# Performance work log

Measured on AMD Instinct MI355X. Metric: run time of the kernel, lower is better.

The kernel has to match this reference:

```python
import jax, jax.numpy as jnp
import numpy as np
import math

B, L, DIM = 2, 2048, 1024
NUM_HEADS, QUANTUM_HEADS, CHUNK = 16, 2, 64
HD = DIM // NUM_HEADS  # 64 == CHUNK (required by the original broadcast)
TH = NUM_HEADS - QUANTUM_HEADS
STEPS = 2048
LN_EPS = 1e-5


def setup_inputs() -> dict:
    key = jax.random.key(0)
    ks = jax.random.split(key, 12)
    inp = {
        'x': jax.random.normal(ks[0], (B, L, DIM), dtype=jnp.float32),
        # to_quantum_state: Linear(HD, 2HD) + LayerNorm(2HD) + Tanh
        'wq1': jax.random.normal(ks[1], (HD, 2 * HD), dtype=jnp.float32) * 0.05,
        'bq1': jnp.zeros((2 * HD,), dtype=jnp.float32),
        'ln_g': jnp.ones((2 * HD,), dtype=jnp.float32),
        'ln_b': jnp.zeros((2 * HD,), dtype=jnp.float32),
        'phase_shifts': jax.random.normal(ks[2], (QUANTUM_HEADS,), dtype=jnp.float32) * 0.02,
        'freqs': jax.random.normal(ks[3], (QUANTUM_HEADS,), dtype=jnp.float32) * 0.02,
        # traditional heads: q/k/v projections, no bias
        'wq': jax.random.normal(ks[4], (DIM, TH * HD), dtype=jnp.float32) * 0.02,
        'wk': jax.random.normal(ks[5], (DIM, TH * HD), dtype=jnp.float32) * 0.02,
        'wv': jax.random.normal(ks[6], (DIM, TH * HD), dtype=jnp.float32) * 0.02,
        # output projection
        'wo': jax.random.normal(ks[7], (DIM, DIM), dtype=jnp.float32) * 0.02,
        'bo': jnp.zeros((DIM,), dtype=jnp.float32),
    }
    return inp


def _quantum_state(t, wq1, bq1, ln_g, ln_b):
    # Linear -> LayerNorm -> Tanh; split into (amp, phase)
    h = t @ wq1 + bq1
    mu = h.mean(-1, keepdims=True)
    var = ((h - mu) ** 2).mean(-1, keepdims=True)
    h = (h - mu) * jax.lax.rsqrt(var + LN_EPS) * ln_g + ln_b
    h = jnp.tanh(h)
    return h[..., :HD], h[..., HD:]


def reference(x, wq1, bq1, ln_g, ln_b, phase_shifts, freqs, wq, wk, wv, wo, bo):
    two_pi = 2.0 * math.pi
    angles = jnp.linspace(0.0, two_pi, STEPS)  # torch.linspace is endpoint-inclusive
    cos_table = jnp.cos(angles)
    inv_sqrt_hd = 1.0 / math.sqrt(HD)
    nc = L // CHUNK

    quantum_outs = []
    for h in range(QUANTUM_HEADS):
        xh = x[..., h * HD:(h + 1) * HD]                       # [B,L,HD]
        amp, phase = _quantum_state(xh, wq1, bq1, ln_g, ln_b)  # each [B,L,HD]
        qa = amp.reshape(B, nc, CHUNK, HD)
        qp = phase.reshape(B, nc, CHUNK, HD)
        # keys/values are truncated to the FIRST `chunk` tokens (original quirk)
        ka = amp[:, :CHUNK]        # [B,CHUNK,HD]
        kp = phase[:, :CHUNK]
        v = xh[:, :CHUNK]
        # phase_diff[b,c,i,j] = qp[b,c,i,j] - kp[b,j,i]  (needs CHUNK == HD)
        pd = (qp - jnp.swapaxes(kp, -1, -2)[:, None]) * freqs[h] + phase_shifts[h]
        idx = jnp.mod(pd / two_pi * STEPS, STEPS).astype(jnp.int32)  # in [0, STEPS)
        interference = cos_table[idx]                          # [B,nc,CHUNK,CHUNK]
        scores = jnp.einsum('bcih,bjh->bcij', qa, ka) * interference
        attn = jax.nn.softmax(scores * inv_sqrt_hd, axis=-1)
        out = jnp.einsum('bcij,bjh->bcih', attn, v).reshape(B, L, HD)
        quantum_outs.append(out)

    # traditional multi-head attention on full x
    q = (x @ wq).reshape(B, L, TH, HD)
    k = (x @ wk).reshape(B, L, TH, HD)
    vv = (x @ wv).reshape(B, L, TH, HD)
    scores = jnp.einsum('bqhd,bkhd->bhqk', q, k) * inv_sqrt_hd
    attn = jax.nn.softmax(scores, axis=-1)
    trad = jnp.einsum('bhqk,bkhd->bqhd', attn, vv).reshape(B, L, TH * HD)

    out = jnp.concatenate(quantum_outs + [trad], axis=-1)  # [B,L,DIM]
    return out @ wo + bo
```

## Files before the change

kernel.cpp:

```cpp
#include <hip/hip_runtime.h>
#include <hip/hip_bf16.h>
#include <math.h>

#define B_ 2
#define L_ 2048
#define DIM_ 1024
#define HD_ 64
#define TH_ 14
#define TWO_PI_F 6.28318530717958647692f
#define QSCALE_F 0.1803368801111204f

typedef __bf16 bf16_t;
typedef __bf16 bf16x8 __attribute__((ext_vector_type(8)));
typedef __bf16 bf16x4 __attribute__((ext_vector_type(4)));
typedef float f32x4 __attribute__((ext_vector_type(4)));
typedef float f32x16 __attribute__((ext_vector_type(16)));
typedef unsigned int u32x2 __attribute__((ext_vector_type(2)));

static __device__ __forceinline__ bf16_t f2b(float f) { return (bf16_t)f; }

static __device__ __forceinline__ float fexp2(float x) {
#if __has_builtin(__builtin_amdgcn_exp2f)
  return __builtin_amdgcn_exp2f(x);
#else
  return exp2f(x);
#endif
}

static __device__ __forceinline__ unsigned int cvtpk(float a, float b) {
  unsigned int r;
  asm("v_cvt_pk_bf16_f32 %0, %1, %2" : "=v"(r) : "v"(a), "v"(b));
  return r;
}

static __device__ __forceinline__ void gl16(const bf16_t* g, bf16_t* l) {
  __builtin_amdgcn_global_load_lds(
      (const __attribute__((address_space(1))) void*)g,
      (__attribute__((address_space(3))) void*)l, 16, 0, 0);
}

static __device__ __forceinline__ void swap32(unsigned int& a, unsigned int& b) {
#if __has_builtin(__builtin_amdgcn_permlane32_swap)
  u32x2 r = __builtin_amdgcn_permlane32_swap(a, b, false, false);
  a = r[0];
  b = r[1];
#else
  const int l = (int)(threadIdx.x & 63);
  unsigned int bp_a = (unsigned int)__builtin_amdgcn_ds_bpermute((l ^ 32) << 2, (int)a);
  unsigned int bp_b = (unsigned int)__builtin_amdgcn_ds_bpermute((l ^ 32) << 2, (int)b);
  unsigned int na = (l < 32) ? a : bp_b;
  unsigned int nb = (l < 32) ? bp_a : b;
  a = na;
  b = nb;
#endif
}

__global__ __launch_bounds__(256)
void k_prep(const float* __restrict__ x, const float* __restrict__ wq1,
            const float* __restrict__ bq1, const float* __restrict__ ln_g,
            const float* __restrict__ ln_b, const float* __restrict__ wq,
            const float* __restrict__ wk, const float* __restrict__ wv,
            const float* __restrict__ wo, bf16_t* __restrict__ xb,
            bf16_t* __restrict__ wt_qkv, bf16_t* __restrict__ wt_o,
            bf16_t* __restrict__ amp_b, float* __restrict__ phase) {
  __shared__ float tile[32][33];
  const int t = threadIdx.x;
  const int bid = blockIdx.x;
  if (bid < 4096) {
    const int i = bid * 256 + t;
    const float4 v4 = ((const float4*)x)[i];
    bf16x4 o = {f2b(v4.x), f2b(v4.y), f2b(v4.z), f2b(v4.w)};
    *(bf16x4*)(xb + 4 * (size_t)i) = o;
  } else if (bid < 7808) {
    const float* W;
    bf16_t* Wt;
    int N, kt, nt;
    if (bid < 6784) {
      int r = bid - 4096;
      const int which = r / 896;
      r -= which * 896;
      W = (which == 0) ? wq : (which == 1) ? wk : wv;
      Wt = wt_qkv + (size_t)which * 896 * 1024;
      N = 896;
      kt = r & 31;
      nt = r >> 5;
    } else {
      const int r = bid - 6784;
      W = wo;
      Wt = wt_o;
      N = 1024;
      kt = r & 31;
      nt = r >> 5;
    }
    const int tx = t & 31, ty = t >> 5;
    const int k0 = kt * 32, n0 = nt * 32;
    #pragma unroll
    for (int i = 0; i < 4; ++i)
      tile[ty + 8 * i][tx] = W[(size_t)(k0 + ty + 8 * i) * N + n0 + tx];
    __syncthreads();
    #pragma unroll
    for (int i = 0; i < 4; ++i)
      Wt[(size_t)(n0 + ty + 8 * i) * 1024 + k0 + tx] = f2b(tile[tx][ty + 8 * i]);
  } else {
    const int gw = ((bid - 7808) * 256 + t) >> 6;
    const int lane = t & 63;
    const int h = gw >> 12;
    const int bl = gw & 4095;
    const float xv = x[(size_t)bl * DIM_ + h * HD_ + lane];
    float acc0 = bq1[lane];
    float acc1 = bq1[64 + lane];
    #pragma unroll 16
    for (int kk = 0; kk < 64; ++kk) {
      const float xk = __shfl(xv, kk, 64);
      acc0 = fmaf(xk, wq1[kk * 128 + lane], acc0);
      acc1 = fmaf(xk, wq1[kk * 128 + 64 + lane], acc1);
    }
    float s = acc0 + acc1;
    #pragma unroll
    for (int off = 32; off > 0; off >>= 1) s += __shfl_xor(s, off, 64);
    const float mu = s * (1.0f / 128.0f);
    const float d0 = acc0 - mu, d1 = acc1 - mu;
    float vsum = d0 * d0 + d1 * d1;
    #pragma unroll
    for (int off = 32; off > 0; off >>= 1) vsum += __shfl_xor(vsum, off, 64);
    const float rstd = rsqrtf(vsum * (1.0f / 128.0f) + 1e-5f);
    const float av = tanhf(d0 * rstd * ln_g[lane] + ln_b[lane]);
    const float pv = tanhf(d1 * rstd * ln_g[64 + lane] + ln_b[64 + lane]);
    const size_t o = ((size_t)h * (B_ * L_) + bl) * HD_ + lane;
    amp_b[o] = f2b(av);
    phase[o] = pv;
  }
}

__global__ __launch_bounds__(256)
void k_mm1q(const bf16_t* __restrict__ A, const bf16_t* __restrict__ Wt,
            bf16_t* __restrict__ qb, bf16_t* __restrict__ kb, bf16_t* __restrict__ vb,
            const bf16_t* __restrict__ amp_b, const float* __restrict__ phase,
            const float* __restrict__ shifts, const float* __restrict__ freqs,
            bf16_t* __restrict__ catb) {
  __shared__ char smem[32768];
  const int t = threadIdx.x;
  const int lane = t & 63, w = t >> 6;
  const int bid = blockIdx.x;
  const int xcd = bid & 7, slot = bid >> 3;
  if (slot < 84) {
    bf16_t* Asm = (bf16_t*)smem;
    bf16_t* Bsm = (bf16_t*)(smem + 16384);
    const int wm = w >> 1, wn = w & 1;
    const int l31 = lane & 31, hi = lane >> 5;
    const int m_blk = xcd * 4 + slot / 21;
    const int n_blk = slot % 21;
    const int m0 = m_blk * 128;
    const int n0 = n_blk * 128;
    f32x16 acc[2][2] = {};
    for (int k0 = 0; k0 < 1024; k0 += 64) {
      __syncthreads();
      #pragma unroll
      for (int qc = 0; qc < 4; ++qc) {
        const int idx = t + 256 * qc;
        const int r = idx >> 3, cb = idx & 7;
        const int c = (cb ^ (r & 7)) * 8;
        gl16(A + (size_t)(m0 + r) * 1024 + k0 + c, Asm + w * 512 + qc * 2048);
        gl16(Wt + (size_t)(n0 + r) * 1024 + k0 + c, Bsm + w * 512 + qc * 2048);
      }
      __syncthreads();
      #pragma unroll
      for (int s = 0; s < 4; ++s) {
        const int ra0 = wm * 64 + l31, ra1 = ra0 + 32;
        const int rb0 = wn * 64 + l31, rb1 = rb0 + 32;
        const bf16x8 af0 = *(const bf16x8*)((char*)Asm + ra0 * 128 + (((2 * s + hi) ^ (ra0 & 7)) << 4));
        const bf16x8 af1 = *(const bf16x8*)((char*)Asm + ra1 * 128 + (((2 * s + hi) ^ (ra1 & 7)) << 4));
        const bf16x8 bf0 = *(const bf16x8*)((char*)Bsm + rb0 * 128 + (((2 * s + hi) ^ (rb0 & 7)) << 4));
        const bf16x8 bf1 = *(const bf16x8*)((char*)Bsm + rb1 * 128 + (((2 * s + hi) ^ (rb1 & 7)) << 4));
        acc[0][0] = __builtin_amdgcn_mfma_f32_32x32x16_bf16(bf0, af0, acc[0][0], 0, 0, 0);
        acc[0][1] = __builtin_amdgcn_mfma_f32_32x32x16_bf16(bf1, af0, acc[0][1], 0, 0, 0);
        acc[1][0] = __builtin_amdgcn_mfma_f32_32x32x16_bf16(bf0, af1, acc[1][0], 0, 0, 0);
        acc[1][1] = __builtin_amdgcn_mfma_f32_32x32x16_bf16(bf1, af1, acc[1][1], 0, 0, 0);
      }
    }
    const int n0w = n0 + wn * 64;
    const int which = (n0 >= 1792) ? 2 : (n0 >= 896) ? 1 : 0;
    #pragma unroll
    for (int mi = 0; mi < 2; ++mi) {
      const int m = m0 + wm * 64 + mi * 32 + l31;
      const int bsel = m >> 11, ll = m & 2047;
      #pragma unroll
      for (int ni = 0; ni < 2; ++ni) {
        if (which == 2) {
          #pragma unroll
          for (int rp = 0; rp < 4; ++rp) {
            #pragma unroll
            for (int e = 0; e < 4; ++e) {
              const int nn = n0w + ni * 32 + 8 * rp + 4 * hi + e - 1792;
              const int head = nn >> 6, hd = nn & 63;
              vb[(((size_t)bsel * TH_ + head) * HD_ + hd) * L_ + ll] = f2b(acc[mi][ni][4 * rp + e]);
            }
          }
        } else {
          const float sc = (which == 0) ? QSCALE_F : 1.0f;
          bf16_t* dst = (which == 0) ? qb : kb;
          #pragma unroll
          for (int rp = 0; rp < 4; ++rp) {
            const int nb = n0w + ni * 32 + 8 * rp + 4 * hi;
            const int nn = nb - which * 896;
            const int head = nn >> 6, hd = nn & 63;
            bf16x4 pk;
            #pragma unroll
            for (int e = 0; e < 4; ++e) pk[e] = f2b(acc[mi][ni][4 * rp + e] * sc);
            *(bf16x4*)(dst + (((size_t)bsel * TH_ + head) * L_ + ll) * HD_ + hd) = pk;
          }
        }
      }
    }
  } else {
    bf16_t* Kam = (bf16_t*)smem;
    bf16_t* Vt  = (bf16_t*)(smem + 8192);
    bf16_t* Ps  = (bf16_t*)(smem + 16384);
    const int l15 = lane & 15, g = lane >> 4;
    const int qv = xcd * 16 + (slot - 84);
    const int c = qv & 31;
    const int hb = qv >> 5;
    const int b = hb & 1;
    const int h = hb >> 1;
    const size_t abase = ((size_t)h * B_ + b) * L_ * HD_;

    {
      const int r0 = t >> 3, cb0 = t & 7;
      const int r1 = r0 + 32;
      gl16(amp_b + abase + r0 * 64 + (cb0 ^ (r0 & 7)) * 8, Kam + w * 512);
      gl16(amp_b + abase + r1 * 64 + (cb0 ^ (r1 & 7)) * 8, Kam + w * 512 + 2048);
    }
    {
      const int vj = t >> 2;
      const int vd0 = (t & 3) * 16;
      const bf16x8 va = *(const bf16x8*)(A + ((size_t)b * L_ + vj) * DIM_ + h * 64 + vd0);
      const bf16x8 vb2 = *(const bf16x8*)(A + ((size_t)b * L_ + vj) * DIM_ + h * 64 + vd0 + 8);
      #pragma unroll
      for (int e = 0; e < 8; ++e) {
        int d = vd0 + e;
        *(bf16_t*)((char*)Vt + d * 128 + (((vj >> 3) ^ (d & 7)) << 4) + (vj & 7) * 2) = va[e];
        d = vd0 + 8 + e;
        *(bf16_t*)((char*)Vt + d * 128 + (((vj >> 3) ^ (d & 7)) << 4) + (vj & 7) * 2) = vb2[e];
      }
    }
    __syncthreads();

    bf16x8 qf[2];
    {
      const size_t ro = abase + (size_t)(c * 64 + 16 * w + l15) * 64 + g * 8;
      qf[0] = *(const bf16x8*)(amp_b + ro);
      qf[1] = *(const bf16x8*)(amp_b + ro + 32);
    }
    f32x4 s[4] = {};
    #pragma unroll
    for (int ks = 0; ks < 2; ++ks) {
      #pragma unroll
      for (int nt = 0; nt < 4; ++nt) {
        const int jr = nt * 16 + l15;
        const bf16x8 kf = *(const bf16x8*)((char*)Kam + jr * 128 + (((ks * 4 + g) ^ (jr & 7)) << 4));
        s[nt] = __builtin_amdgcn_mfma_f32_16x16x32_bf16(qf[ks], kf, s[nt], 0, 0, 0);
      }
    }
    const float freq = freqs[h], shift = shifts[h];
    char* PsW = (char*)Ps + w * 2048;
    float l_acc[4];
    #pragma unroll
    for (int r = 0; r < 4; ++r) {
      const int i_loc = 16 * w + 4 * g + r;
      const float* qrow = phase + abase + (size_t)(c * 64 + i_loc) * 64;
      const float* krow = phase + abase + i_loc;
      const int row = g * 4 + r;
      float ls = 0.0f;
      #pragma unroll
      for (int nt = 0; nt < 4; ++nt) {
        const int j = nt * 16 + l15;
        const float qp = qrow[j];
        const float kp = krow[j * 64];
        const float pd = (qp - kp) * freq + shift;
        const float t1 = pd * (2048.0f / TWO_PI_F);
        float mm = fmodf(t1, 2048.0f);
        if (mm < 0.0f) mm += 2048.0f;
        int idx = (int)mm;
        idx = idx > 2047 ? 2047 : idx;
        const float interf = cosf((float)idx * (TWO_PI_F / 2047.0f));
        const float sc = s[nt][r] * interf * 0.125f;
        const float e = expf(sc);
        ls += e;
        *(bf16_t*)(PsW + row * 128 + (((j >> 3) ^ (row & 7)) << 4) + (j & 7) * 2) = f2b(e);
      }
      #pragma unroll
      for (int off = 1; off < 16; off <<= 1) ls += __shfl_xor(ls, off, 64);
      l_acc[r] = ls;
    }
    f32x4 o[4] = {};
    #pragma unroll
    for (int ks = 0; ks < 2; ++ks) {
      const bf16x8 pa = *(const bf16x8*)(PsW + l15 * 128 + (((ks * 4 + g) ^ (l15 & 7)) << 4));
      #pragma unroll
      for (int nt = 0; nt < 4; ++nt) {
        const int dr = nt * 16 + l15;
        const bf16x8 vf = *(const bf16x8*)((char*)Vt + dr * 128 + (((ks * 4 + g) ^ (dr & 7)) << 4));
        o[nt] = __builtin_amdgcn_mfma_f32_16x16x32_bf16(pa, vf, o[nt], 0, 0, 0);
      }
    }
    #pragma unroll
    for (int r = 0; r < 4; ++r) {
      const float inv = 1.0f / l_acc[r];
      const int qrow = c * 64 + 16 * w + g * 4 + r;
      #pragma unroll
      for (int nt = 0; nt < 4; ++nt)
        catb[((size_t)b * L_ + qrow) * DIM_ + h * 64 + nt * 16 + l15] = f2b(o[nt][r] * inv);
    }
  }
}

__global__ __launch_bounds__(256)
void k_mm0(const bf16_t* __restrict__ A, const bf16_t* __restrict__ Wt,
           const float* __restrict__ bias, float* __restrict__ outf) {
  __shared__ bf16_t Asm[128 * 64];
  __shared__ bf16_t Bsm[128 * 64];
  const int t = threadIdx.x;
  const int lane = t & 63, w = t >> 6;
  const int wm = w >> 1, wn = w & 1;
  const int l31 = lane & 31, hi = lane >> 5;
  const int bid = blockIdx.x;
  const int v = (bid & 7) * 32 + (bid >> 3);
  const int m0 = (v & 31) * 128;
  const int n0 = (v >> 5) * 128;
  f32x16 acc[2][2] = {};
  for (int k0 = 0; k0 < 1024; k0 += 64) {
    __syncthreads();
    #pragma unroll
    for (int qc = 0; qc < 4; ++qc) {
      const int idx = t + 256 * qc;
      const int r = idx >> 3, cb = idx & 7;
      const int c = (cb ^ (r & 7)) * 8;
      gl16(A + (size_t)(m0 + r) * 1024 + k0 + c, Asm + w * 512 + qc * 2048);
      gl16(Wt + (size_t)(n0 + r) * 1024 + k0 + c, Bsm + w * 512 + qc * 2048);
    }
    __syncthreads();
    #pragma unroll
    for (int s = 0; s < 4; ++s) {
      const int ra0 = wm * 64 + l31, ra1 = ra0 + 32;
      const int rb0 = wn * 64 + l31, rb1 = rb0 + 32;
      const bf16x8 af0 = *(const bf16x8*)((char*)Asm + ra0 * 128 + (((2 * s + hi) ^ (ra0 & 7)) << 4));
      const bf16x8 af1 = *(const bf16x8*)((char*)Asm + ra1 * 128 + (((2 * s + hi) ^ (ra1 & 7)) << 4));
      const bf16x8 bf0 = *(const bf16x8*)((char*)Bsm + rb0 * 128 + (((2 * s + hi) ^ (rb0 & 7)) << 4));
      const bf16x8 bf1 = *(const bf16x8*)((char*)Bsm + rb1 * 128 + (((2 * s + hi) ^ (rb1 & 7)) << 4));
      acc[0][0] = __builtin_amdgcn_mfma_f32_32x32x16_bf16(bf0, af0, acc[0][0], 0, 0, 0);
      acc[0][1] = __builtin_amdgcn_mfma_f32_32x32x16_bf16(bf1, af0, acc[0][1], 0, 0, 0);
      acc[1][0] = __builtin_amdgcn_mfma_f32_32x32x16_bf16(bf0, af1, acc[1][0], 0, 0, 0);
      acc[1][1] = __builtin_amdgcn_mfma_f32_32x32x16_bf16(bf1, af1, acc[1][1], 0, 0, 0);
    }
  }
  #pragma unroll
  for (int mi = 0; mi < 2; ++mi) {
    const int m = m0 + wm * 64 + mi * 32 + l31;
    #pragma unroll
    for (int ni = 0; ni < 2; ++ni) {
      #pragma unroll
      for (int rp = 0; rp < 4; ++rp) {
        const int nb = n0 + wn * 64 + ni * 32 + 8 * rp + 4 * hi;
        const float4 bv = *(const float4*)&bias[nb];
        float4 r4;
        r4.x = acc[mi][ni][4 * rp + 0] + bv.x;
        r4.y = acc[mi][ni][4 * rp + 1] + bv.y;
        r4.z = acc[mi][ni][4 * rp + 2] + bv.z;
        r4.w = acc[mi][ni][4 * rp + 3] + bv.w;
        *(float4*)&outf[(size_t)m * 1024 + nb] = r4;
      }
    }
  }
}

__global__ __launch_bounds__(512)
void k_flash2(const bf16_t* __restrict__ qg, const bf16_t* __restrict__ kg,
              const bf16_t* __restrict__ vt, bf16_t* __restrict__ catb) {
  __shared__ char smem[65536];
  const int t = threadIdx.x;
  const int lane = t & 63, w = t >> 6;
  const int g2 = w >> 2, wl = w & 3;
  const int l31 = lane & 31, hi = lane >> 5;
  int bid = blockIdx.x;
  bid = (bid & 7) * 56 + (bid >> 3);
  const int qblk = bid & 15, bh = bid >> 4;
  const int head = bh % TH_, b = bh / TH_;
  const size_t base = (size_t)bh * (L_ * HD_);
  const int q = qblk * 128 + wl * 32 + l31;
  const int tl = t & 255;
  const int r0 = tl >> 3, cb0 = tl & 7;
  const int r1 = r0 + 32;
  const int c0 = (cb0 ^ (r0 & 7)) * 8;
  const int c1 = (cb0 ^ (r1 & 7)) * 8;
  const int ubase = wl * 512;
  bf16_t* Kg = (bf16_t*)(smem + g2 * 32768);
  bf16_t* Vg = (bf16_t*)(smem + g2 * 32768 + 16384);
  const int kt0 = g2 * 16;

  bf16x8 qf[4];
  #pragma unroll
  for (int slot = 0; slot < 4; ++slot)
    qf[slot] = *(const bf16x8*)(qg + base + (size_t)q * 64 + 16 * slot + 8 * hi);

  f32x16 oT[2] = {};
  float l_acc = 0.0f;

  {
    const bf16_t* ksrc = kg + base + (size_t)kt0 * 64 * 64;
    const bf16_t* vsrc = vt + base + kt0 * 64;
    gl16(ksrc + r0 * 64 + c0, Kg + ubase);
    gl16(ksrc + r1 * 64 + c1, Kg + ubase + 2048);
    gl16(vsrc + (size_t)r0 * L_ + c0, Vg + ubase);
    gl16(vsrc + (size_t)r1 * L_ + c1, Vg + ubase + 2048);
  }
  for (int kt = 0; kt < 16; ++kt) {
    const int cur = kt & 1;
    if (kt < 15) {
      const bf16_t* ksrc = kg + base + (size_t)(kt0 + kt + 1) * 64 * 64;
      const bf16_t* vsrc = vt + base + (kt0 + kt + 1) * 64;
      bf16_t* kd = Kg + (cur ^ 1) * 4096;
      bf16_t* vd = Vg + (cur ^ 1) * 4096;
      gl16(ksrc + r0 * 64 + c0, kd + ubase);
      gl16(ksrc + r1 * 64 + c1, kd + ubase + 2048);
      gl16(vsrc + (size_t)r0 * L_ + c0, vd + ubase);
      gl16(vsrc + (size_t)r1 * L_ + c1, vd + ubase + 2048);
      asm volatile("s_waitcnt vmcnt(4)" ::: "memory");
    } else {
      asm volatile("s_waitcnt vmcnt(0)" ::: "memory");
    }
    __builtin_amdgcn_sched_barrier(0);
    __builtin_amdgcn_s_barrier();
    const char* Kc = (const char*)(Kg + cur * 4096);
    const char* Vc = (const char*)(Vg + cur * 4096);
    f32x16 sT0 = {}, sT1 = {};
    __builtin_amdgcn_s_setprio(1);
    #pragma unroll
    for (int slot = 0; slot < 4; ++slot) {
      const int row0 = l31;
      const int row1 = 32 + l31;
      const bf16x8 kf0 = *(const bf16x8*)(Kc + row0 * 128 + (((2 * slot + hi) ^ (row0 & 7)) << 4));
      const bf16x8 kf1 = *(const bf16x8*)(Kc + row1 * 128 + (((2 * slot + hi) ^ (row1 & 7)) << 4));
      sT0 = __builtin_amdgcn_mfma_f32_32x32x16_bf16(kf0, qf[slot], sT0, 0, 0, 0);
      sT1 = __builtin_amdgcn_mfma_f32_32x32x16_bf16(kf1, qf[slot], sT1, 0, 0, 0);
    }
    __builtin_amdgcn_s_setprio(0);
    unsigned int W0[8], W1[8];
    float la = 0.0f;
    #pragma unroll
    for (int rp = 0; rp < 8; ++rp) {
      const float p00 = fexp2(sT0[2 * rp]);
      const float p01 = fexp2(sT0[2 * rp + 1]);
      const float p10 = fexp2(sT1[2 * rp]);
      const float p11 = fexp2(sT1[2 * rp + 1]);
      la += (p00 + p01) + (p10 + p11);
      W0[rp] = cvtpk(p00, p01);
      W1[rp] = cvtpk(p10, p11);
    }
    l_acc += la;
    unsigned int pb[4][4];
    #pragma unroll
    for (int m1 = 0; m1 < 2; ++m1) {
      unsigned int u, vv;
      u = W0[m1];     vv = W0[2 + m1]; swap32(u, vv); pb[0][m1] = u; pb[0][m1 + 2] = vv;
      u = W0[4 + m1]; vv = W0[6 + m1]; swap32(u, vv); pb[1][m1] = u; pb[1][m1 + 2] = vv;
      u = W1[m1];     vv = W1[2 + m1]; swap32(u, vv); pb[2][m1] = u; pb[2][m1 + 2] = vv;
      u = W1[4 + m1]; vv = W1[6 + m1]; swap32(u, vv); pb[3][m1] = u; pb[3][m1 + 2] = vv;
    }
    __builtin_amdgcn_s_setprio(1);
    #pragma unroll
    for (int slot = 0; slot < 4; ++slot) {
      union { unsigned int u[4]; bf16x8 v8; } pf;
      pf.u[0] = pb[slot][0]; pf.u[1] = pb[slot][1];
      pf.u[2] = pb[slot][2]; pf.u[3] = pb[slot][3];
      #pragma unroll
      for (int dt = 0; dt < 2; ++dt) {
        const int row = 32 * dt + l31;
        const bf16x8 vf = *(const bf16x8*)(Vc + row * 128 + (((2 * slot + hi) ^ (row & 7)) << 4));
        oT[dt] = __builtin_amdgcn_mfma_f32_32x32x16_bf16(vf, pf.v8, oT[dt], 0, 0, 0);
      }
    }
    __builtin_amdgcn_s_setprio(0);
    __builtin_amdgcn_s_barrier();
  }
  const float l_w = l_acc + __shfl_xor(l_acc, 32, 64);
  __syncthreads();
  float* obuf = (float*)(smem + 32768);
  float* lbuf = (float*)smem;
  if (g2 == 1) {
    #pragma unroll
    for (int dt = 0; dt < 2; ++dt)
      #pragma unroll
      for (int e = 0; e < 16; ++e)
        obuf[(dt * 16 + e) * 256 + wl * 64 + lane] = oT[dt][e];
    lbuf[wl * 64 + lane] = l_w;
  }
  __syncthreads();
  if (g2 == 0) {
    const float l_tot = l_w + lbuf[wl * 64 + lane];
    const float inv = 1.0f / l_tot;
    const size_t obase = ((size_t)b * L_ + q) * DIM_ + 128 + head * 64;
    #pragma unroll
    for (int dt = 0; dt < 2; ++dt) {
      #pragma unroll
      for (int rq = 0; rq < 4; ++rq) {
        bf16x4 pk;
        #pragma unroll
        for (int e = 0; e < 4; ++e)
          pk[e] = f2b((oT[dt][4 * rq + e] +
                       obuf[(dt * 16 + 4 * rq + e) * 256 + wl * 64 + lane]) * inv);
        *(bf16x4*)(catb + obase + 32 * dt + 8 * rq + 4 * hi) = pk;
      }
    }
  }
}

extern "C" void kernel_launch(void* const* d_in, const int* in_sizes, int n_in,
                              void* d_out, int out_size, void* d_ws, size_t ws_size,
                              hipStream_t stream) {
  (void)in_sizes; (void)n_in; (void)out_size; (void)ws_size;
  const float* x      = (const float*)d_in[0];
  const float* wq1    = (const float*)d_in[1];
  const float* bq1    = (const float*)d_in[2];
  const float* ln_g   = (const float*)d_in[3];
  const float* ln_b   = (const float*)d_in[4];
  const float* shifts = (const float*)d_in[5];
  const float* freqs  = (const float*)d_in[6];
  const float* wq     = (const float*)d_in[7];
  const float* wk     = (const float*)d_in[8];
  const float* wv     = (const float*)d_in[9];
  const float* wo     = (const float*)d_in[10];
  const float* bo     = (const float*)d_in[11];
  float* out = (float*)d_out;

  char* p = (char*)d_ws;
  bf16_t* amp_b  = (bf16_t*)p; p += (size_t)2 * B_ * L_ * HD_ * 2;
  float* phase   = (float*)p;  p += (size_t)2 * B_ * L_ * HD_ * 4;
  bf16_t* xb     = (bf16_t*)p; p += (size_t)B_ * L_ * DIM_ * 2;
  bf16_t* wt_qkv = (bf16_t*)p; p += (size_t)2688 * 1024 * 2;
  bf16_t* wt_o   = (bf16_t*)p; p += (size_t)1024 * 1024 * 2;
  bf16_t* qb     = (bf16_t*)p; p += (size_t)B_ * TH_ * L_ * HD_ * 2;
  bf16_t* kb     = (bf16_t*)p; p += (size_t)B_ * TH_ * L_ * HD_ * 2;
  bf16_t* vtb    = (bf16_t*)p; p += (size_t)B_ * TH_ * L_ * HD_ * 2;
  bf16_t* catb   = (bf16_t*)p;

  k_prep<<<dim3(9856), dim3(256), 0, stream>>>(x, wq1, bq1, ln_g, ln_b,
                                               wq, wk, wv, wo,
                                               xb, wt_qkv, wt_o, amp_b, phase);
  k_mm1q<<<dim3(800), dim3(256), 0, stream>>>(xb, wt_qkv, qb, kb, vtb,
                                              amp_b, phase, shifts, freqs, catb);
  k_flash2<<<dim3(448), dim3(512), 0, stream>>>(qb, kb, vtb, catb);
  k_mm0<<<dim3(256), dim3(256), 0, stream>>>(catb, wt_o, bo, out);
}
```

Baseline: 121.0 us.

## Move quantum-head attention blocks from QKV GEMM kernel into flash kernel

The chunked quantum-head attention work, previously run as 128 extra blocks of the QKV projection GEMM kernel, now runs inside the flash-attention kernel as 64 extra 512-thread blocks, each doing two chunks with one 256-thread group per chunk. The GEMM kernel becomes a pure GEMM with 672 blocks, and the flash kernel grows from 448 to 512 blocks. The goal is to rebalance load: the GEMM grid shrinks and the small quantum blocks fill idle CUs during flash attention rather than competing with GEMM tiles. The risk is that quantum blocks in the flash grid occupy 512-thread slots and extend the flash kernel's tail.

```diff
diff --git a/kernel.cpp b/kernel.cpp
--- a/kernel.cpp
+++ b/kernel.cpp
@@ -134,182 +134,78 @@
 
 __global__ __launch_bounds__(256)
 void k_mm1q(const bf16_t* __restrict__ A, const bf16_t* __restrict__ Wt,
-            bf16_t* __restrict__ qb, bf16_t* __restrict__ kb, bf16_t* __restrict__ vb,
-            const bf16_t* __restrict__ amp_b, const float* __restrict__ phase,
-            const float* __restrict__ shifts, const float* __restrict__ freqs,
-            bf16_t* __restrict__ catb) {
+            bf16_t* __restrict__ qb, bf16_t* __restrict__ kb, bf16_t* __restrict__ vb) {
   __shared__ char smem[32768];
   const int t = threadIdx.x;
   const int lane = t & 63, w = t >> 6;
   const int bid = blockIdx.x;
   const int xcd = bid & 7, slot = bid >> 3;
-  if (slot < 84) {
-    bf16_t* Asm = (bf16_t*)smem;
-    bf16_t* Bsm = (bf16_t*)(smem + 16384);
-    const int wm = w >> 1, wn = w & 1;
-    const int l31 = lane & 31, hi = lane >> 5;
-    const int m_blk = xcd * 4 + slot / 21;
-    const int n_blk = slot % 21;
-    const int m0 = m_blk * 128;
-    const int n0 = n_blk * 128;
-    f32x16 acc[2][2] = {};
-    for (int k0 = 0; k0 < 1024; k0 += 64) {
-      __syncthreads();
-      #pragma unroll
-      for (int qc = 0; qc < 4; ++qc) {
-        const int idx = t + 256 * qc;
-        const int r = idx >> 3, cb = idx & 7;
-        const int c = (cb ^ (r & 7)) * 8;
-        gl16(A + (size_t)(m0 + r) * 1024 + k0 + c, Asm + w * 512 + qc * 2048);
-        gl16(Wt + (size_t)(n0 + r) * 1024 + k0 + c, Bsm + w * 512 + qc * 2048);
-      }
-      __syncthreads();
-      #pragma unroll
-      for (int s = 0; s < 4; ++s) {
-        const int ra0 = wm * 64 + l31, ra1 = ra0 + 32;
-        const int rb0 = wn * 64 + l31, rb1 = rb0 + 32;
-        const bf16x8 af0 = *(const bf16x8*)((char*)Asm + ra0 * 128 + (((2 * s + hi) ^ (ra0 & 7)) << 4));
-        const bf16x8 af1 = *(const bf16x8*)((char*)Asm + ra1 * 128 + (((2 * s + hi) ^ (ra1 & 7)) << 4));
-        const bf16x8 bf0 = *(const bf16x8*)((char*)Bsm + rb0 * 128 + (((2 * s + hi) ^ (rb0 & 7)) << 4));
-        const bf16x8 bf1 = *(const bf16x8*)((char*)Bsm + rb1 * 128 + (((2 * s + hi) ^ (rb1 & 7)) << 4));
-        acc[0][0] = __builtin_amdgcn_mfma_f32_32x32x16_bf16(bf0, af0, acc[0][0], 0, 0, 0);
-        acc[0][1] = __builtin_amdgcn_mfma_f32_32x32x16_bf16(bf1, af0, acc[0][1], 0, 0, 0);
-        acc[1][0] = __builtin_amdgcn_mfma_f32_32x32x16_bf16(bf0, af1, acc[1][0], 0, 0, 0);
-        acc[1][1] = __builtin_amdgcn_mfma_f32_32x32x16_bf16(bf1, af1, acc[1][1], 0, 0, 0);
-      }
-    }
-    const int n0w = n0 + wn * 64;
-    const int which = (n0 >= 1792) ? 2 : (n0 >= 896) ? 1 : 0;
-    #pragma unroll
-    for (int mi = 0; mi < 2; ++mi) {
-      const int m = m0 + wm * 64 + mi * 32 + l31;
-      const int bsel = m >> 11, ll = m & 2047;
-      #pragma unroll
-      for (int ni = 0; ni < 2; ++ni) {
-        if (which == 2) {
+  bf16_t* Asm = (bf16_t*)smem;
+  bf16_t* Bsm = (bf16_t*)(smem + 16384);
+  const int wm = w >> 1, wn = w & 1;
+  const int l31 = lane & 31, hi = lane >> 5;
+  const int m_blk = xcd * 4 + slot / 21;
+  const int n_blk = slot % 21;
+  const int m0 = m_blk * 128;
+  const int n0 = n_blk * 128;
+  f32x16 acc[2][2] = {};
+  for (int k0 = 0; k0 < 1024; k0 += 64) {
+    __syncthreads();
+    #pragma unroll
+    for (int qc = 0; qc < 4; ++qc) {
+      const int idx = t + 256 * qc;
+      const int r = idx >> 3, cb = idx & 7;
+      const int c = (cb ^ (r & 7)) * 8;
+      gl16(A + (size_t)(m0 + r) * 1024 + k0 + c, Asm + w * 512 + qc * 2048);
+      gl16(Wt + (size_t)(n0 + r) * 1024 + k0 + c, Bsm + w * 512 + qc * 2048);
+    }
+    __syncthreads();
+    #pragma unroll
+    for (int s = 0; s < 4; ++s) {
+      const int ra0 = wm * 64 + l31, ra1 = ra0 + 32;
+      const int rb0 = wn * 64 + l31, rb1 = rb0 + 32;
+      const bf16x8 af0 = *(const bf16x8*)((char*)Asm + ra0 * 128 + (((2 * s + hi) ^ (ra0 & 7)) << 4));
+      const bf16x8 af1 = *(const bf16x8*)((char*)Asm + ra1 * 128 + (((2 * s + hi) ^ (ra1 & 7)) << 4));
+      const bf16x8 bf0 = *(const bf16x8*)((char*)Bsm + rb0 * 128 + (((2 * s + hi) ^ (rb0 & 7)) << 4));
+      const bf16x8 bf1 = *(const bf16x8*)((char*)Bsm + rb1 * 128 + (((2 * s + hi) ^ (rb1 & 7)) << 4));
+      acc[0][0] = __builtin_amdgcn_mfma_f32_32x32x16_bf16(bf0, af0, acc[0][0], 0, 0, 0);
+      acc[0][1] = __builtin_amdgcn_mfma_f32_32x32x16_bf16(bf1, af0, acc[0][1], 0, 0, 0);
+      acc[1][0] = __builtin_amdgcn_mfma_f32_32x32x16_bf16(bf0, af1, acc[1][0], 0, 0, 0);
+      acc[1][1] = __builtin_amdgcn_mfma_f32_32x32x16_bf16(bf1, af1, acc[1][1], 0, 0, 0);
+    }
+  }
+  const int n0w = n0 + wn * 64;
+  const int which = (n0 >= 1792) ? 2 : (n0 >= 896) ? 1 : 0;
+  #pragma unroll
+  for (int mi = 0; mi < 2; ++mi) {
+    const int m = m0 + wm * 64 + mi * 32 + l31;
+    const int bsel = m >> 11, ll = m & 2047;
+    #pragma unroll
+    for (int ni = 0; ni < 2; ++ni) {
+      if (which == 2) {
+        #pragma unroll
+        for (int rp = 0; rp < 4; ++rp) {
           #pragma unroll
-          for (int rp = 0; rp < 4; ++rp) {
-            #pragma unroll
-            for (int e = 0; e < 4; ++e) {
-              const int nn = n0w + ni * 32 + 8 * rp + 4 * hi + e - 1792;
-              const int head = nn >> 6, hd = nn & 63;
-              vb[(((size_t)bsel * TH_ + head) * HD_ + hd) * L_ + ll] = f2b(acc[mi][ni][4 * rp + e]);
-            }
-          }
-        } else {
-          const float sc = (which == 0) ? QSCALE_F : 1.0f;
-          bf16_t* dst = (which == 0) ? qb : kb;
-          #pragma unroll
-          for (int rp = 0; rp < 4; ++rp) {
-            const int nb = n0w + ni * 32 + 8 * rp + 4 * hi;
-            const int nn = nb - which * 896;
+          for (int e = 0; e < 4; ++e) {
+            const int nn = n0w + ni * 32 + 8 * rp + 4 * hi + e - 1792;
             const int head = nn >> 6, hd = nn & 63;
-            bf16x4 pk;
-            #pragma unroll
-            for (int e = 0; e < 4; ++e) pk[e] = f2b(acc[mi][ni][4 * rp + e] * sc);
-            *(bf16x4*)(dst + (((size_t)bsel * TH_ + head) * L_ + ll) * HD_ + hd) = pk;
+            vb[(((size_t)bsel * TH_ + head) * HD_ + hd) * L_ + ll] = f2b(acc[mi][ni][4 * rp + e]);
           }
         }
-      }
-    }
-  } else {
-    bf16_t* Kam = (bf16_t*)smem;
-    bf16_t* Vt  = (bf16_t*)(smem + 8192);
-    bf16_t* Ps  = (bf16_t*)(smem + 16384);
-    const int l15 = lane & 15, g = lane >> 4;
-    const int qv = xcd * 16 + (slot - 84);
-    const int c = qv & 31;
-    const int hb = qv >> 5;
-    const int b = hb & 1;
-    const int h = hb >> 1;
-    const size_t abase = ((size_t)h * B_ + b) * L_ * HD_;
-
-    {
-      const int r0 = t >> 3, cb0 = t & 7;
-      const int r1 = r0 + 32;
-      gl16(amp_b + abase + r0 * 64 + (cb0 ^ (r0 & 7)) * 8, Kam + w * 512);
-      gl16(amp_b + abase + r1 * 64 + (cb0 ^ (r1 & 7)) * 8, Kam + w * 512 + 2048);
-    }
-    {
-      const int vj = t >> 2;
-      const int vd0 = (t & 3) * 16;
-      const bf16x8 va = *(const bf16x8*)(A + ((size_t)b * L_ + vj) * DIM_ + h * 64 + vd0);
-      const bf16x8 vb2 = *(const bf16x8*)(A + ((size_t)b * L_ + vj) * DIM_ + h * 64 + vd0 + 8);
-      #pragma unroll
-      for (int e = 0; e < 8; ++e) {
-        int d = vd0 + e;
-        *(bf16_t*)((char*)Vt + d * 128 + (((vj >> 3) ^ (d & 7)) << 4) + (vj & 7) * 2) = va[e];
-        d = vd0 + 8 + e;
-        *(bf16_t*)((char*)Vt + d * 128 + (((vj >> 3) ^ (d & 7)) << 4) + (vj & 7) * 2) = vb2[e];
-      }
-    }
-    __syncthreads();
-
-    bf16x8 qf[2];
-    {
-      const size_t ro = abase + (size_t)(c * 64 + 16 * w + l15) * 64 + g * 8;
-      qf[0] = *(const bf16x8*)(amp_b + ro);
-      qf[1] = *(const bf16x8*)(amp_b + ro + 32);
-    }
-    f32x4 s[4] = {};
-    #pragma unroll
-    for (int ks = 0; ks < 2; ++ks) {
-      #pragma unroll
-      for (int nt = 0; nt < 4; ++nt) {
-        const int jr = nt * 16 + l15;
-        const bf16x8 kf = *(const bf16x8*)((char*)Kam + jr * 128 + (((ks * 4 + g) ^ (jr & 7)) << 4));
-        s[nt] = __builtin_amdgcn_mfma_f32_16x16x32_bf16(qf[ks], kf, s[nt], 0, 0, 0);
-      }
-    }
-    const float freq = freqs[h], shift = shifts[h];
-    char* PsW = (char*)Ps + w * 2048;
-    float l_acc[4];
-    #pragma unroll
-    for (int r = 0; r < 4; ++r) {
-      const int i_loc = 16 * w + 4 * g + r;
-      const float* qrow = phase + abase + (size_t)(c * 64 + i_loc) * 64;
-      const float* krow = phase + abase + i_loc;
-      const int row = g * 4 + r;
-      float ls = 0.0f;
-      #pragma unroll
-      for (int nt = 0; nt < 4; ++nt) {
-        const int j = nt * 16 + l15;
-        const float qp = qrow[j];
-        const float kp = krow[j * 64];
-        const float pd = (qp - kp) * freq + shift;
-        const float t1 = pd * (2048.0f / TWO_PI_F);
-        float mm = fmodf(t1, 2048.0f);
-        if (mm < 0.0f) mm += 2048.0f;
-        int idx = (int)mm;
-        idx = idx > 2047 ? 2047 : idx;
-        const float interf = cosf((float)idx * (TWO_PI_F / 2047.0f));
-        const float sc = s[nt][r] * interf * 0.125f;
-        const float e = expf(sc);
-        ls += e;
-        *(bf16_t*)(PsW + row * 128 + (((j >> 3) ^ (row & 7)) << 4) + (j & 7) * 2) = f2b(e);
-      }
-      #pragma unroll
-      for (int off = 1; off < 16; off <<= 1) ls += __shfl_xor(ls, off, 64);
-      l_acc[r] = ls;
-    }
-    f32x4 o[4] = {};
-    #pragma unroll
-    for (int ks = 0; ks < 2; ++ks) {
-      const bf16x8 pa = *(const bf16x8*)(PsW + l15 * 128 + (((ks * 4 + g) ^ (l15 & 7)) << 4));
-      #pragma unroll
-      for (int nt = 0; nt < 4; ++nt) {
-        const int dr = nt * 16 + l15;
-        const bf16x8 vf = *(const bf16x8*)((char*)Vt + dr * 128 + (((ks * 4 + g) ^ (dr & 7)) << 4));
-        o[nt] = __builtin_amdgcn_mfma_f32_16x16x32_bf16(pa, vf, o[nt], 0, 0, 0);
-      }
-    }
-    #pragma unroll
-    for (int r = 0; r < 4; ++r) {
-      const float inv = 1.0f / l_acc[r];
-      const int qrow = c * 64 + 16 * w + g * 4 + r;
-      #pragma unroll
-      for (int nt = 0; nt < 4; ++nt)
-        catb[((size_t)b * L_ + qrow) * DIM_ + h * 64 + nt * 16 + l15] = f2b(o[nt][r] * inv);
+      } else {
+        const float sc = (which == 0) ? QSCALE_F : 1.0f;
+        bf16_t* dst = (which == 0) ? qb : kb;
+        #pragma unroll
+        for (int rp = 0; rp < 4; ++rp) {
+          const int nb = n0w + ni * 32 + 8 * rp + 4 * hi;
+          const int nn = nb - which * 896;
+          const int head = nn >> 6, hd = nn & 63;
+          bf16x4 pk;
+          #pragma unroll
+          for (int e = 0; e < 4; ++e) pk[e] = f2b(acc[mi][ni][4 * rp + e] * sc);
+          *(bf16x4*)(dst + (((size_t)bsel * TH_ + head) * L_ + ll) * HD_ + hd) = pk;
+        }
+      }
     }
   }
 }
@@ -375,141 +271,248 @@
 
 __global__ __launch_bounds__(512)
 void k_flash2(const bf16_t* __restrict__ qg, const bf16_t* __restrict__ kg,
-              const bf16_t* __restrict__ vt, bf16_t* __restrict__ catb) {
+              const bf16_t* __restrict__ vt, bf16_t* __restrict__ catb,
+              const bf16_t* __restrict__ A, const bf16_t* __restrict__ amp_b,
+              const float* __restrict__ phase, const float* __restrict__ shifts,
+              const float* __restrict__ freqs) {
   __shared__ char smem[65536];
   const int t = threadIdx.x;
   const int lane = t & 63, w = t >> 6;
-  const int g2 = w >> 2, wl = w & 3;
   const int l31 = lane & 31, hi = lane >> 5;
-  int bid = blockIdx.x;
-  bid = (bid & 7) * 56 + (bid >> 3);
-  const int qblk = bid & 15, bh = bid >> 4;
-  const int head = bh % TH_, b = bh / TH_;
-  const size_t base = (size_t)bh * (L_ * HD_);
-  const int q = qblk * 128 + wl * 32 + l31;
-  const int tl = t & 255;
-  const int r0 = tl >> 3, cb0 = tl & 7;
-  const int r1 = r0 + 32;
-  const int c0 = (cb0 ^ (r0 & 7)) * 8;
-  const int c1 = (cb0 ^ (r1 & 7)) * 8;
-  const int ubase = wl * 512;
-  bf16_t* Kg = (bf16_t*)(smem + g2 * 32768);
-  bf16_t* Vg = (bf16_t*)(smem + g2 * 32768 + 16384);
-  const int kt0 = g2 * 16;
-
-  bf16x8 qf[4];
-  #pragma unroll
-  for (int slot = 0; slot < 4; ++slot)
-    qf[slot] = *(const bf16x8*)(qg + base + (size_t)q * 64 + 16 * slot + 8 * hi);
-
-  f32x16 oT[2] = {};
-  float l_acc = 0.0f;
-
-  {
-    const bf16_t* ksrc = kg + base + (size_t)kt0 * 64 * 64;
-    const bf16_t* vsrc = vt + base + kt0 * 64;
-    gl16(ksrc + r0 * 64 + c0, Kg + ubase);
-    gl16(ksrc + r1 * 64 + c1, Kg + ubase + 2048);
-    gl16(vsrc + (size_t)r0 * L_ + c0, Vg + ubase);
-    gl16(vsrc + (size_t)r1 * L_ + c1, Vg + ubase + 2048);
-  }
-  for (int kt = 0; kt < 16; ++kt) {
-    const int cur = kt & 1;
-    if (kt < 15) {
-      const bf16_t* ksrc = kg + base + (size_t)(kt0 + kt + 1) * 64 * 64;
-      const bf16_t* vsrc = vt + base + (kt0 + kt + 1) * 64;
-      bf16_t* kd = Kg + (cur ^ 1) * 4096;
-      bf16_t* vd = Vg + (cur ^ 1) * 4096;
-      gl16(ksrc + r0 * 64 + c0, kd + ubase);
-      gl16(ksrc + r1 * 64 + c1, kd + ubase + 2048);
-      gl16(vsrc + (size_t)r0 * L_ + c0, vd + ubase);
-      gl16(vsrc + (size_t)r1 * L_ + c1, vd + ubase + 2048);
-      asm volatile("s_waitcnt vmcnt(4)" ::: "memory");
-    } else {
-      asm volatile("s_waitcnt vmcnt(0)" ::: "memory");
-    }
-    __builtin_amdgcn_sched_barrier(0);
-    __builtin_amdgcn_s_barrier();
-    const char* Kc = (const char*)(Kg + cur * 4096);
-    const char* Vc = (const char*)(Vg + cur * 4096);
-    f32x16 sT0 = {}, sT1 = {};
-    __builtin_amdgcn_s_setprio(1);
-    #pragma unroll
-    for (int slot = 0; slot < 4; ++slot) {
-      const int row0 = l31;
-      const int row1 = 32 + l31;
-      const bf16x8 kf0 = *(const bf16x8*)(Kc + row0 * 128 + (((2 * slot + hi) ^ (row0 & 7)) << 4));
-      const bf16x8 kf1 = *(const bf16x8*)(Kc + row1 * 128 + (((2 * slot + hi) ^ (row1 & 7)) << 4));
-      sT0 = __builtin_amdgcn_mfma_f32_32x32x16_bf16(kf0, qf[slot], sT0, 0, 0, 0);
-      sT1 = __builtin_amdgcn_mfma_f32_32x32x16_bf16(kf1, qf[slot], sT1, 0, 0, 0);
-    }
-    __builtin_amdgcn_s_setprio(0);
-    unsigned int W0[8], W1[8];
-    float la = 0.0f;
-    #pragma unroll
-    for (int rp = 0; rp < 8; ++rp) {
-      const float p00 = fexp2(sT0[2 * rp]);
-      const float p01 = fexp2(sT0[2 * rp + 1]);
-      const float p10 = fexp2(sT1[2 * rp]);
-      const float p11 = fexp2(sT1[2 * rp + 1]);
-      la += (p00 + p01) + (p10 + p11);
-      W0[rp] = cvtpk(p00, p01);
-      W1[rp] = cvtpk(p10, p11);
-    }
-    l_acc += la;
-    unsigned int pb[4][4];
-    #pragma unroll
-    for (int m1 = 0; m1 < 2; ++m1) {
-      unsigned int u, vv;
-      u = W0[m1];     vv = W0[2 + m1]; swap32(u, vv); pb[0][m1] = u; pb[0][m1 + 2] = vv;
-      u = W0[4 + m1]; vv = W0[6 + m1]; swap32(u, vv); pb[1][m1] = u; pb[1][m1 + 2] = vv;
-      u = W1[m1];     vv = W1[2 + m1]; swap32(u, vv); pb[2][m1] = u; pb[2][m1 + 2] = vv;
-      u = W1[4 + m1]; vv = W1[6 + m1]; swap32(u, vv); pb[3][m1] = u; pb[3][m1 + 2] = vv;
-    }
-    __builtin_amdgcn_s_setprio(1);
-    #pragma unroll
-    for (int slot = 0; slot < 4; ++slot) {
-      union { unsigned int u[4]; bf16x8 v8; } pf;
-      pf.u[0] = pb[slot][0]; pf.u[1] = pb[slot][1];
-      pf.u[2] = pb[slot][2]; pf.u[3] = pb[slot][3];
+  const int xcd = blockIdx.x & 7, s = blockIdx.x >> 3;
+  if (s < 56) {
+    const int g2 = w >> 2, wl = w & 3;
+    const int tb = xcd * 56 + s;
+    const int qblk = tb & 15, bh = tb >> 4;
+    const int head = bh % TH_, b = bh / TH_;
+    const size_t base = (size_t)bh * (L_ * HD_);
+    const int q = qblk * 128 + wl * 32 + l31;
+    const int tl = t & 255;
+    const int r0 = tl >> 3, cb0 = tl & 7;
+    const int r1 = r0 + 32;
+    const int c0 = (cb0 ^ (r0 & 7)) * 8;
+    const int c1 = (cb0 ^ (r1 & 7)) * 8;
+    const int ubase = wl * 512;
+    bf16_t* Kg = (bf16_t*)(smem + g2 * 32768);
+    bf16_t* Vg = (bf16_t*)(smem + g2 * 32768 + 16384);
+    const int kt0 = g2 * 16;
+
+    bf16x8 qf[4];
+    #pragma unroll
+    for (int slot = 0; slot < 4; ++slot)
+      qf[slot] = *(const bf16x8*)(qg + base + (size_t)q * 64 + 16 * slot + 8 * hi);
+
+    f32x16 oT[2] = {};
+    float l_acc = 0.0f;
+
+    {
+      const bf16_t* ksrc = kg + base + (size_t)kt0 * 64 * 64;
+      const bf16_t* vsrc = vt + base + kt0 * 64;
+      gl16(ksrc + r0 * 64 + c0, Kg + ubase);
+      gl16(ksrc + r1 * 64 + c1, Kg + ubase + 2048);
+      gl16(vsrc + (size_t)r0 * L_ + c0, Vg + ubase);
+      gl16(vsrc + (size_t)r1 * L_ + c1, Vg + ubase + 2048);
+    }
+    for (int kt = 0; kt < 16; ++kt) {
+      const int cur = kt & 1;
+      if (kt < 15) {
+        const bf16_t* ksrc = kg + base + (size_t)(kt0 + kt + 1) * 64 * 64;
+        const bf16_t* vsrc = vt + base + (kt0 + kt + 1) * 64;
+        bf16_t* kd = Kg + (cur ^ 1) * 4096;
+        bf16_t* vd = Vg + (cur ^ 1) * 4096;
+        gl16(ksrc + r0 * 64 + c0, kd + ubase);
+        gl16(ksrc + r1 * 64 + c1, kd + ubase + 2048);
+        gl16(vsrc + (size_t)r0 * L_ + c0, vd + ubase);
+        gl16(vsrc + (size_t)r1 * L_ + c1, vd + ubase + 2048);
+        asm volatile("s_waitcnt vmcnt(4)" ::: "memory");
+      } else {
+        asm volatile("s_waitcnt vmcnt(0)" ::: "memory");
+      }
+      __builtin_amdgcn_sched_barrier(0);
+      __builtin_amdgcn_s_barrier();
+      const char* Kc = (const char*)(Kg + cur * 4096);
+      const char* Vc = (const char*)(Vg + cur * 4096);
+      f32x16 sT0 = {}, sT1 = {};
+      __builtin_amdgcn_s_setprio(1);
+      #pragma unroll
+      for (int slot = 0; slot < 4; ++slot) {
+        const int row0 = l31;
+        const int row1 = 32 + l31;
+        const bf16x8 kf0 = *(const bf16x8*)(Kc + row0 * 128 + (((2 * slot + hi) ^ (row0 & 7)) << 4));
+        const bf16x8 kf1 = *(const bf16x8*)(Kc + row1 * 128 + (((2 * slot + hi) ^ (row1 & 7)) << 4));
+        sT0 = __builtin_amdgcn_mfma_f32_32x32x16_bf16(kf0, qf[slot], sT0, 0, 0, 0);
+        sT1 = __builtin_amdgcn_mfma_f32_32x32x16_bf16(kf1, qf[slot], sT1, 0, 0, 0);
+      }
+      __builtin_amdgcn_s_setprio(0);
+      unsigned int W0[8], W1[8];
+      float la = 0.0f;
+      #pragma unroll
+      for (int rp = 0; rp < 8; ++rp) {
+        const float p00 = fexp2(sT0[2 * rp]);
+        const float p01 = fexp2(sT0[2 * rp + 1]);
+        const float p10 = fexp2(sT1[2 * rp]);
+        const float p11 = fexp2(sT1[2 * rp + 1]);
+        la += (p00 + p01) + (p10 + p11);
+        W0[rp] = cvtpk(p00, p01);
+        W1[rp] = cvtpk(p10, p11);
+      }
+      l_acc += la;
+      unsigned int pb[4][4];
+      #pragma unroll
+      for (int m1 = 0; m1 < 2; ++m1) {
+        unsigned int u, vv;
+        u = W0[m1];     vv = W0[2 + m1]; swap32(u, vv); pb[0][m1] = u; pb[0][m1 + 2] = vv;
+        u = W0[4 + m1]; vv = W0[6 + m1]; swap32(u, vv); pb[1][m1] = u; pb[1][m1 + 2] = vv;
+        u = W1[m1];     vv = W1[2 + m1]; swap32(u, vv); pb[2][m1] = u; pb[2][m1 + 2] = vv;
+        u = W1[4 + m1]; vv = W1[6 + m1]; swap32(u, vv); pb[3][m1] = u; pb[3][m1 + 2] = vv;
+      }
+      __builtin_amdgcn_s_setprio(1);
+      #pragma unroll
+      for (int slot = 0; slot < 4; ++slot) {
+        union { unsigned int u[4]; bf16x8 v8; } pf;
+        pf.u[0] = pb[slot][0]; pf.u[1] = pb[slot][1];
+        pf.u[2] = pb[slot][2]; pf.u[3] = pb[slot][3];
+        #pragma unroll
+        for (int dt = 0; dt < 2; ++dt) {
+          const int row = 32 * dt + l31;
+          const bf16x8 vf = *(const bf16x8*)(Vc + row * 128 + (((2 * slot + hi) ^ (row & 7)) << 4));
+          oT[dt] = __builtin_amdgcn_mfma_f32_32x32x16_bf16(vf, pf.v8, oT[dt], 0, 0, 0);
+        }
+      }
+      __builtin_amdgcn_s_setprio(0);
+      __builtin_amdgcn_s_barrier();
+    }
+    const float l_w = l_acc + __shfl_xor(l_acc, 32, 64);
+    __syncthreads();
+    float* obuf = (float*)(smem + 32768);
+    float* lbuf = (float*)smem;
+    if (g2 == 1) {
+      #pragma unroll
+      for (int dt = 0; dt < 2; ++dt)
+        #pragma unroll
+        for (int e = 0; e < 16; ++e)
+          obuf[(dt * 16 + e) * 256 + wl * 64 + lane] = oT[dt][e];
+      lbuf[wl * 64 + lane] = l_w;
+    }
+    __syncthreads();
+    if (g2 == 0) {
+      const float l_tot = l_w + lbuf[wl * 64 + lane];
+      const float inv = 1.0f / l_tot;
+      const size_t obase = ((size_t)b * L_ + q) * DIM_ + 128 + head * 64;
       #pragma unroll
       for (int dt = 0; dt < 2; ++dt) {
-        const int row = 32 * dt + l31;
-        const bf16x8 vf = *(const bf16x8*)(Vc + row * 128 + (((2 * slot + hi) ^ (row & 7)) << 4));
-        oT[dt] = __builtin_amdgcn_mfma_f32_32x32x16_bf16(vf, pf.v8, oT[dt], 0, 0, 0);
-      }
-    }
-    __builtin_amdgcn_s_setprio(0);
-    __builtin_amdgcn_s_barrier();
-  }
-  const float l_w = l_acc + __shfl_xor(l_acc, 32, 64);
-  __syncthreads();
-  float* obuf = (float*)(smem + 32768);
-  float* lbuf = (float*)smem;
-  if (g2 == 1) {
-    #pragma unroll
-    for (int dt = 0; dt < 2; ++dt)
-      #pragma unroll
-      for (int e = 0; e < 16; ++e)
-        obuf[(dt * 16 + e) * 256 + wl * 64 + lane] = oT[dt][e];
-    lbuf[wl * 64 + lane] = l_w;
-  }
-  __syncthreads();
-  if (g2 == 0) {
-    const float l_tot = l_w + lbuf[wl * 64 + lane];
-    const float inv = 1.0f / l_tot;
-    const size_t obase = ((size_t)b * L_ + q) * DIM_ + 128 + head * 64;
-    #pragma unroll
-    for (int dt = 0; dt < 2; ++dt) {
-      #pragma unroll
-      for (int rq = 0; rq < 4; ++rq) {
-        bf16x4 pk;
         #pragma unroll
-        for (int e = 0; e < 4; ++e)
-          pk[e] = f2b((oT[dt][4 * rq + e] +
-                       obuf[(dt * 16 + 4 * rq + e) * 256 + wl * 64 + lane]) * inv);
-        *(bf16x4*)(catb + obase + 32 * dt + 8 * rq + 4 * hi) = pk;
-      }
+        for (int rq = 0; rq < 4; ++rq) {
+          bf16x4 pk;
+          #pragma unroll
+          for (int e = 0; e < 4; ++e)
+            pk[e] = f2b((oT[dt][4 * rq + e] +
+                         obuf[(dt * 16 + 4 * rq + e) * 256 + wl * 64 + lane]) * inv);
+          *(bf16x4*)(catb + obase + 32 * dt + 8 * rq + 4 * hi) = pk;
+        }
+      }
+    }
+  } else {
+    const int g3 = w >> 2, wl = w & 3;
+    const int tl = t & 255;
+    bf16_t* Kam = (bf16_t*)(smem + g3 * 24576);
+    bf16_t* Vt2 = (bf16_t*)(smem + g3 * 24576 + 8192);
+    bf16_t* Ps  = (bf16_t*)(smem + g3 * 24576 + 16384);
+    const int l15 = lane & 15, g = lane >> 4;
+    const int qp = xcd * 8 + (s - 56);
+    const int qv = qp * 2 + g3;
+    const int c = qv & 31;
+    const int hb = qv >> 5;
+    const int b = hb & 1;
+    const int h = hb >> 1;
+    const size_t abase = ((size_t)h * B_ + b) * L_ * HD_;
+
+    {
+      const int r0 = tl >> 3, cb0 = tl & 7;
+      const int r1 = r0 + 32;
+      gl16(amp_b + abase + r0 * 64 + (cb0 ^ (r0 & 7)) * 8, Kam + wl * 512);
+      gl16(amp_b + abase + r1 * 64 + (cb0 ^ (r1 & 7)) * 8, Kam + wl * 512 + 2048);
+    }
+    {
+      const int vj = tl >> 2;
+      const int vd0 = (tl & 3) * 16;
+      const bf16x8 va = *(const bf16x8*)(A + ((size_t)b * L_ + vj) * DIM_ + h * 64 + vd0);
+      const bf16x8 vb2 = *(const bf16x8*)(A + ((size_t)b * L_ + vj) * DIM_ + h * 64 + vd0 + 8);
+      #pragma unroll
+      for (int e = 0; e < 8; ++e) {
+        int d = vd0 + e;
+        *(bf16_t*)((char*)Vt2 + d * 128 + (((vj >> 3) ^ (d & 7)) << 4) + (vj & 7) * 2) = va[e];
+        d = vd0 + 8 + e;
+        *(bf16_t*)((char*)Vt2 + d * 128 + (((vj >> 3) ^ (d & 7)) << 4) + (vj & 7) * 2) = vb2[e];
+      }
+    }
+    __syncthreads();
+
+    bf16x8 qf[2];
+    {
+      const size_t ro = abase + (size_t)(c * 64 + 16 * wl + l15) * 64 + g * 8;
+      qf[0] = *(const bf16x8*)(amp_b + ro);
+      qf[1] = *(const bf16x8*)(amp_b + ro + 32);
+    }
+    f32x4 sq[4] = {};
+    #pragma unroll
+    for (int ks = 0; ks < 2; ++ks) {
+      #pragma unroll
+      for (int nt = 0; nt < 4; ++nt) {
+        const int jr = nt * 16 + l15;
+        const bf16x8 kf = *(const bf16x8*)((char*)Kam + jr * 128 + (((ks * 4 + g) ^ (jr & 7)) << 4));
+        sq[nt] = __builtin_amdgcn_mfma_f32_16x16x32_bf16(qf[ks], kf, sq[nt], 0, 0, 0);
+      }
+    }
+    const float freq = freqs[h], shift = shifts[h];
+    char* PsW = (char*)Ps + wl * 2048;
+    float l_acc[4];
+    #pragma unroll
+    for (int r = 0; r < 4; ++r) {
+      const int i_loc = 16 * wl + 4 * g + r;
+      const float* qrow = phase + abase + (size_t)(c * 64 + i_loc) * 64;
+      const float* krow = phase + abase + i_loc;
+      const int row = g * 4 + r;
+      float ls = 0.0f;
+      #pragma unroll
+      for (int nt = 0; nt < 4; ++nt) {
+        const int j = nt * 16 + l15;
+        const float qp2 = qrow[j];
+        const float kp = krow[j * 64];
+        const float pd = (qp2 - kp) * freq + shift;
+        const float t1 = pd * (2048.0f / TWO_PI_F);
+        float mm = fmodf(t1, 2048.0f);
+        if (mm < 0.0f) mm += 2048.0f;
+        int idx = (int)mm;
+        idx = idx > 2047 ? 2047 : idx;
+        const float interf = cosf((float)idx * (TWO_PI_F / 2047.0f));
+        const float sc = sq[nt][r] * interf * 0.125f;
+        const float e = expf(sc);
+        ls += e;
+        *(bf16_t*)(PsW + row * 128 + (((j >> 3) ^ (row & 7)) << 4) + (j & 7) * 2) = f2b(e);
+      }
+      #pragma unroll
+      for (int off = 1; off < 16; off <<= 1) ls += __shfl_xor(ls, off, 64);
+      l_acc[r] = ls;
+    }
+    f32x4 o[4] = {};
+    #pragma unroll
+    for (int ks = 0; ks < 2; ++ks) {
+      const bf16x8 pa = *(const bf16x8*)(PsW + l15 * 128 + (((ks * 4 + g) ^ (l15 & 7)) << 4));
+      #pragma unroll
+      for (int nt = 0; nt < 4; ++nt) {
+        const int dr = nt * 16 + l15;
+        const bf16x8 vf = *(const bf16x8*)((char*)Vt2 + dr * 128 + (((ks * 4 + g) ^ (dr & 7)) << 4));
+        o[nt] = __builtin_amdgcn_mfma_f32_16x16x32_bf16(pa, vf, o[nt], 0, 0, 0);
+      }
+    }
+    #pragma unroll
+    for (int r = 0; r < 4; ++r) {
+      const float inv = 1.0f / l_acc[r];
+      const int qrow = c * 64 + 16 * wl + g * 4 + r;
+      #pragma unroll
+      for (int nt = 0; nt < 4; ++nt)
+        catb[((size_t)b * L_ + qrow) * DIM_ + h * 64 + nt * 16 + l15] = f2b(o[nt][r] * inv);
     }
   }
 }
@@ -546,8 +549,8 @@
   k_prep<<<dim3(9856), dim3(256), 0, stream>>>(x, wq1, bq1, ln_g, ln_b,
                                                wq, wk, wv, wo,
                                                xb, wt_qkv, wt_o, amp_b, phase);
-  k_mm1q<<<dim3(800), dim3(256), 0, stream>>>(xb, wt_qkv, qb, kb, vtb,
-                                              amp_b, phase, shifts, freqs, catb);
-  k_flash2<<<dim3(448), dim3(512), 0, stream>>>(qb, kb, vtb, catb);
+  k_mm1q<<<dim3(672), dim3(256), 0, stream>>>(xb, wt_qkv, qb, kb, vtb);
+  k_flash2<<<dim3(512), dim3(512), 0, stream>>>(qb, kb, vtb, catb,
+                                                xb, amp_b, phase, shifts, freqs);
   k_mm0<<<dim3(256), dim3(256), 0, stream>>>(catb, wt_o, bo, out);
 }
```

Measured after the change: 119.9 us. Within noise of the previous version (-0.8%).
